# Optimization experiments

Measured on AMD Instinct MI355X. Metric: run time of the kernel, lower is better.

The kernel has to match this reference:

```python
import jax, jax.numpy as jnp
import numpy as np

N, H, B, E = 8192, 64, 8, 262144


def setup_inputs() -> dict:
    key = jax.random.key(0)
    ks = jax.random.split(key, 16)
    inp = {
        "x": jax.random.uniform(ks[0], (B, N, 2), dtype=jnp.float32),
        "edge_index": jax.random.randint(ks[1], (2, E), 0, N, dtype=jnp.int64),
        "target_node": jax.random.randint(ks[2], (B,), 0, N, dtype=jnp.int64),
        "current_prereq_mask": jax.random.uniform(ks[3], (B, N), dtype=jnp.float32),
        # learned parameters (eval mode: dropout is identity)
        "node_emb": jax.random.normal(ks[4], (N, H), dtype=jnp.float32) * 0.02,
        "W_sp": jax.random.normal(ks[5], (H, 2), dtype=jnp.float32) * 0.5,
        "b_sp": jnp.zeros((H,), dtype=jnp.float32),
        "W_g": jax.random.normal(ks[6], (H, H), dtype=jnp.float32) * (1.0 / np.sqrt(H)),
        "b_g": jnp.zeros((H,), dtype=jnp.float32),
        "W_d": jax.random.normal(ks[7], (1, H), dtype=jnp.float32) * (1.0 / np.sqrt(H)),
        "b_d": jnp.zeros((1,), dtype=jnp.float32),
        "W_a": jax.random.normal(ks[8], (1, H), dtype=jnp.float32) * (1.0 / np.sqrt(H)),
        "b_a": jnp.zeros((1,), dtype=jnp.float32),
        "prereq_w": jnp.array([1.0], dtype=jnp.float32),
    }
    return inp


def _build_adj_norm(edge_index):
    # A_hat = A + I ; adj_norm = D^{-1/2} A_hat D^{-1/2}, dense [N, N]
    adj = jnp.zeros((N, N), dtype=jnp.float32).at[edge_index[0], edge_index[1]].set(1.0)
    adj = adj + jnp.eye(N, dtype=jnp.float32)
    deg = adj.sum(axis=1)
    dis = jnp.where(deg > 0, deg ** -0.5, 0.0)
    return dis[:, None] * adj * dis[None, :]


def reference(x, edge_index, target_node, current_prereq_mask,
              node_emb, W_sp, b_sp, W_g, b_g, W_d, b_d, W_a, b_a, prereq_w):
    adj_norm = _build_adj_norm(edge_index)               # [N, N]
    h = node_emb[None] + x @ W_sp.T + b_sp               # [B, N, H]
    h_proj = h @ W_g.T                                   # [B, N, H]
    z = jnp.einsum('nm,bmh->bnh', adj_norm, h_proj) + b_g
    z = jax.nn.relu(z)                                   # [B, N, H]

    target_emb = jnp.take_along_axis(z, target_node[:, None, None].astype(jnp.int32).repeat(1, axis=1), axis=1)[:, 0, :]  # [B, H]
    difficulty = (target_emb @ W_d.T + b_d)[:, 0]        # [B]

    scores = x[:, :, 1]                                  # [B, N]
    n_learned = jnp.clip(x[:, :, 0].sum(axis=1), 1.0)    # [B]
    weighted_z = jnp.einsum('bnh,bn->bh', z, scores) / n_learned[:, None]
    ability = (weighted_z @ W_a.T + b_a)[:, 0]           # [B]

    z_pos = jax.nn.softplus(z)
    prereq_agg = jnp.einsum('bnh,bn->bh', z_pos, current_prereq_mask).mean(axis=-1)  # [B]
    prereq_strength = jnp.abs(prereq_w)[0] * prereq_agg

    gap = ability - difficulty + prereq_strength
    prob = jax.nn.sigmoid(gap)
    return prob, gap
```

## Files before the change

### kernel.cpp

```cpp
#include <hip/hip_runtime.h>
#include <hip/hip_bf16.h>
#include <math.h>

#define N 8192
#define H 64
#define B 8
#define MAXDEG 128
#define REPS 32
#define RPW 2

#define OFF_MASK 0ULL
#define OFF_CNT  8388608ULL
#define OFF_WR   8421376ULL
#define OFF_PR   8486912ULL
#define OFF_NL   8552448ULL
#define ZERO_END 8552512ULL
#define OFF_COLS 8552512ULL
#define OFF_TGT  10649664ULL
#define OFF_UV   10651712ULL
#define OFF_XD   10652480ULL
#define OFF_PD   11701056ULL

__device__ __forceinline__ float bf2f(unsigned short u) {
    return __uint_as_float(((unsigned)u) << 16);
}

__global__ __launch_bounds__(256) void k_zero(float4* __restrict__ p) {
    unsigned i = blockIdx.x * 256u + threadIdx.x;
    if (i < (unsigned)(ZERO_END / 16))
        p[i] = make_float4(0.f, 0.f, 0.f, 0.f);
}

__global__ __launch_bounds__(256) void k_edges(const int* __restrict__ ei, int nE,
                                               unsigned* __restrict__ bits,
                                               unsigned* __restrict__ cnt,
                                               unsigned short* __restrict__ cols) {
    int e = blockIdx.x * blockDim.x + threadIdx.x;
    if (e >= nE) return;
    int r = ei[e];
    int c = ei[nE + e];
    unsigned bitidx = (unsigned)r * (unsigned)N + (unsigned)c;
    unsigned bit = 1u << (bitidx & 31u);
    unsigned old = atomicOr(&bits[bitidx >> 5], bit);
    if (!(old & bit)) {
        unsigned k = atomicAdd(&cnt[r], 1u);
        if (k < MAXDEG) cols[r * MAXDEG + k] = (unsigned short)c;
    }
}

__global__ __launch_bounds__(256) void k_prepxd(const float* __restrict__ ne,
                                                const float* __restrict__ W_g,
                                                const float* __restrict__ W_sp,
                                                const float* __restrict__ b_sp,
                                                const float* __restrict__ x,
                                                const float* __restrict__ pmask,
                                                const unsigned* __restrict__ cnt,
                                                __hip_bfloat16* __restrict__ Pd,
                                                float* __restrict__ uvec,
                                                float* __restrict__ xd,
                                                float* __restrict__ nlacc) {
    __shared__ float wgs[H * 65];
    __shared__ __align__(16) float hv[16 * H];
    const int tid = threadIdx.x, lane = tid & 63, wv = tid >> 6;
    const int bid = blockIdx.x;

    if (bid < 512) {
        for (int e = tid; e < H * H; e += 256)
            wgs[(e >> 6) * 65 + (e & 63)] = W_g[e];
        const float* nebase = ne + (size_t)bid * 16 * H;
        for (int j = 0; j < 4; ++j) {
            int e = tid + j * 256;
            hv[e] = nebase[e];
        }
        __syncthreads();
        float wr[H];
#pragma unroll
        for (int k = 0; k < H; ++k) wr[k] = wgs[lane * 65 + k];

        if (bid == 0 && wv == 0) {
            float v0 = W_sp[lane * 2 + 0], v1 = W_sp[lane * 2 + 1], vb = b_sp[lane];
            float a0 = 0.f, a1 = 0.f, a2 = 0.f;
#pragma unroll
            for (int k = 0; k < H; ++k) {
                a0 = fmaf(wr[k], __shfl(v0, k, 64), a0);
                a1 = fmaf(wr[k], __shfl(v1, k, 64), a1);
                a2 = fmaf(wr[k], __shfl(vb, k, 64), a2);
            }
            uvec[lane] = a0; uvec[64 + lane] = a1; uvec[128 + lane] = a2;
        }

        for (int ii = 0; ii < 4; ++ii) {
            const int node = wv * 4 + ii;
            const int m = bid * 16 + node;
            const float4* h4p = (const float4*)&hv[node * H];
            float acc = 0.f;
#pragma unroll
            for (int kk = 0; kk < 16; ++kk) {
                float4 h4 = h4p[kk];
                acc = fmaf(wr[4 * kk + 0], h4.x, acc);
                acc = fmaf(wr[4 * kk + 1], h4.y, acc);
                acc = fmaf(wr[4 * kk + 2], h4.z, acc);
                acc = fmaf(wr[4 * kk + 3], h4.w, acc);
            }
            float dis = rsqrtf((float)(cnt[m] + 1u));
            Pd[m * H + lane] = __float2bfloat16(dis * acc);
        }
    } else {
        const int m = (bid - 512) * 256 + tid;
        float dis = rsqrtf((float)(cnt[m] + 1u));
        float row[32];
#pragma unroll
        for (int j = 0; j < 32; ++j) row[j] = 0.f;
        row[16] = dis;
#pragma unroll
        for (int b = 0; b < B; ++b) {
            float2 xv = ((const float2*)x)[b * N + m];
            row[b]      = dis * xv.x;
            row[8 + b]  = dis * xv.y;
            row[17 + b] = pmask[b * N + m];
            float s = xv.x;
            for (int off = 32; off; off >>= 1) s += __shfl_down(s, off, 64);
            if (lane == 0) atomicAdd(&nlacc[b], s);
        }
        float4* dst = (float4*)&xd[m * 32];
#pragma unroll
        for (int j = 0; j < 8; ++j)
            dst[j] = make_float4(row[4 * j], row[4 * j + 1], row[4 * j + 2], row[4 * j + 3]);
    }
}

__global__ __launch_bounds__(256) void k_spmm(const unsigned short* __restrict__ Pd,
                                              const float* __restrict__ xd,
                                              const unsigned* __restrict__ cnt,
                                              const unsigned short* __restrict__ cols,
                                              const float* __restrict__ uvec,
                                              const float* __restrict__ b_g,
                                              const int* __restrict__ target,
                                              float* __restrict__ wr_,
                                              float* __restrict__ pr_,
                                              float* __restrict__ tgt) {
    const int lane = threadIdx.x & 63;
    const int wv = threadIdx.x >> 6;
    const int wid = blockIdx.x * 4 + wv;
    const float u0 = uvec[lane], u1 = uvec[64 + lane], ub = uvec[128 + lane];
    const float bg = b_g[lane];
    int tg[B];
#pragma unroll
    for (int b = 0; b < B; ++b) tg[b] = target[b];
    float wa[B], pa[B];
#pragma unroll
    for (int b = 0; b < B; ++b) { wa[b] = 0.f; pa[b] = 0.f; }

    for (int i = 0; i < RPW; ++i) {
        const int r = wid * RPW + i;
        float rloc = xd[r * 32 + (lane & 31)];
        float sp = bf2f(Pd[r * H + lane]);
        float sx = rloc;
        const int kc = min((int)cnt[r], MAXDEG);
        const unsigned short* cl = &cols[r * MAXDEG];
#pragma unroll 4
        for (int k = 0; k < kc; ++k) {
            int c = (int)cl[k];
            sp += bf2f(Pd[c * H + lane]);
            sx += xd[c * 32 + (lane & 31)];
        }
        const float dis_r = __shfl(rloc, 16, 64);
        const float rdis = 1.0f / dis_r;
        const float sd = __shfl(sx, 16, 64);
        const float base = fmaf(sd, ub, sp);
#pragma unroll
        for (int b = 0; b < B; ++b) {
            float sx0 = __shfl(sx, b, 64);
            float sx1 = __shfl(sx, 8 + b, 64);
            float sc  = __shfl(rloc, 8 + b, 64) * rdis;
            float mk  = __shfl(rloc, 17 + b, 64);
            float v = fmaf(sx0, u0, fmaf(sx1, u1, base));
            float z = fmaxf(fmaf(dis_r, v, bg), 0.f);
            wa[b] = fmaf(z, sc, wa[b]);
            float spl = z + __logf(1.f + __expf(-z));
            pa[b] = fmaf(spl, mk, pa[b]);
            if (r == tg[b]) tgt[b * H + lane] = z;
        }
    }
    const int rep = wid & (REPS - 1);
#pragma unroll
    for (int b = 0; b < B; ++b) {
        atomicAdd(&wr_[(rep * B + b) * H + lane], wa[b]);
        atomicAdd(&pr_[(rep * B + b) * H + lane], pa[b]);
    }
}

__global__ __launch_bounds__(512) void k_final(const float* __restrict__ wr_,
                                               const float* __restrict__ pr_,
                                               const float* __restrict__ nlacc,
                                               const float* __restrict__ tgt,
                                               const float* __restrict__ W_d,
                                               const float* __restrict__ b_d,
                                               const float* __restrict__ W_a,
                                               const float* __restrict__ b_a,
                                               const float* __restrict__ prereq_w,
                                               float* __restrict__ out) {
    int tid = threadIdx.x, b = tid >> 6, h = tid & 63;
    float ws = 0.f, ps = 0.f;
#pragma unroll 8
    for (int rep = 0; rep < REPS; ++rep) {
        ws += wr_[(rep * B + b) * H + h];
        ps += pr_[(rep * B + b) * H + h];
    }
    float nl = fmaxf(nlacc[b], 1.0f);
    float ap = (ws / nl) * W_a[h];
    float dp = tgt[b * H + h] * W_d[h];
    float pp = ps;
    for (int off = 32; off; off >>= 1) {
        ap += __shfl_down(ap, off, 64);
        dp += __shfl_down(dp, off, 64);
        pp += __shfl_down(pp, off, 64);
    }
    if (h == 0) {
        float ability    = ap + b_a[0];
        float difficulty = dp + b_d[0];
        float preq       = fabsf(prereq_w[0]) * (pp * (1.0f / (float)H));
        float gap  = ability - difficulty + preq;
        float prob = 1.0f / (1.0f + __expf(-gap));
        out[b]     = prob;
        out[B + b] = gap;
    }
}

extern "C" void kernel_launch(void* const* d_in, const int* in_sizes, int n_in,
                              void* d_out, int out_size, void* d_ws, size_t ws_size,
                              hipStream_t stream) {
    const float* x        = (const float*)d_in[0];
    const int*   ei       = (const int*)d_in[1];
    const int*   target   = (const int*)d_in[2];
    const float* pmask    = (const float*)d_in[3];
    const float* node_emb = (const float*)d_in[4];
    const float* W_sp     = (const float*)d_in[5];
    const float* b_sp     = (const float*)d_in[6];
    const float* W_g      = (const float*)d_in[7];
    const float* b_g      = (const float*)d_in[8];
    const float* W_d      = (const float*)d_in[9];
    const float* b_d      = (const float*)d_in[10];
    const float* W_a      = (const float*)d_in[11];
    const float* b_a      = (const float*)d_in[12];
    const float* prereq_w = (const float*)d_in[13];

    const int nE = in_sizes[1] / 2;

    char* ws = (char*)d_ws;
    unsigned*        bits = (unsigned*)(ws + OFF_MASK);
    unsigned*        cnt  = (unsigned*)(ws + OFF_CNT);
    float*           wr_  = (float*)(ws + OFF_WR);
    float*           pr_  = (float*)(ws + OFF_PR);
    float*           nlac = (float*)(ws + OFF_NL);
    unsigned short*  cols = (unsigned short*)(ws + OFF_COLS);
    float*           tgt  = (float*)(ws + OFF_TGT);
    float*           uvec = (float*)(ws + OFF_UV);
    float*           xd   = (float*)(ws + OFF_XD);
    __hip_bfloat16*  Pd   = (__hip_bfloat16*)(ws + OFF_PD);

    k_zero<<<(unsigned)(ZERO_END / 16 + 255) / 256, 256, 0, stream>>>((float4*)ws);
    k_edges<<<(nE + 255) / 256, 256, 0, stream>>>(ei, nE, bits, cnt, cols);
    k_prepxd<<<544, 256, 0, stream>>>(node_emb, W_g, W_sp, b_sp, x, pmask, cnt,
                                      Pd, uvec, xd, nlac);
    k_spmm<<<N / (4 * RPW), 256, 0, stream>>>((const unsigned short*)Pd, xd, cnt, cols,
                                              uvec, b_g, target, wr_, pr_, tgt);
    k_final<<<1, 512, 0, stream>>>(wr_, pr_, nlac, tgt, W_d, b_d, W_a, b_a,
                                   prereq_w, (float*)d_out);
}
```

Baseline: 79.16 us.

## Fuse all stages into one persistent kernel with software grid barriers

Replaces the five separate launches (zero, edge insertion, prep, spmm, final) with a single 512-block persistent kernel that separates phases with atomic-counter grid barriers, plus a tiny kernel that resets the barrier counters. The goal is to remove per-launch overhead and the inter-kernel gaps. The partial-sum replica count drops from 32 to 16, and the final reduction is done by block 0 after a completion counter. This relies on all 512 blocks being co-resident, since the spin barriers could deadlock otherwise, and each barrier adds sleep/poll latency.

```diff
diff --git a/kernel.cpp b/kernel.cpp
--- a/kernel.cpp
+++ b/kernel.cpp
@@ -6,73 +6,104 @@
 #define H 64
 #define B 8
 #define MAXDEG 128
-#define REPS 32
-#define RPW 2
+#define REPS 16
+#define NBLK 512
+#define NTHR 256
+#define GSIZE (NBLK * NTHR)
+#define NWAVE (NBLK * 4)
+#define RPW   (N / NWAVE)
 
 #define OFF_MASK 0ULL
 #define OFF_CNT  8388608ULL
 #define OFF_WR   8421376ULL
-#define OFF_PR   8486912ULL
-#define OFF_NL   8552448ULL
-#define ZERO_END 8552512ULL
-#define OFF_COLS 8552512ULL
-#define OFF_TGT  10649664ULL
-#define OFF_UV   10651712ULL
-#define OFF_XD   10652480ULL
-#define OFF_PD   11701056ULL
+#define OFF_PR   8454144ULL
+#define OFF_NL   8486912ULL
+#define ZERO_END 8486976ULL
+#define OFF_BAR  8486976ULL
+#define OFF_COLS 8487040ULL
+#define OFF_TGT  10584192ULL
+#define OFF_UV   10586240ULL
+#define OFF_XD   10587008ULL
+#define OFF_PD   11635584ULL
 
 __device__ __forceinline__ float bf2f(unsigned short u) {
     return __uint_as_float(((unsigned)u) << 16);
 }
 
-__global__ __launch_bounds__(256) void k_zero(float4* __restrict__ p) {
-    unsigned i = blockIdx.x * 256u + threadIdx.x;
-    if (i < (unsigned)(ZERO_END / 16))
-        p[i] = make_float4(0.f, 0.f, 0.f, 0.f);
-}
-
-__global__ __launch_bounds__(256) void k_edges(const int* __restrict__ ei, int nE,
-                                               unsigned* __restrict__ bits,
-                                               unsigned* __restrict__ cnt,
-                                               unsigned short* __restrict__ cols) {
-    int e = blockIdx.x * blockDim.x + threadIdx.x;
-    if (e >= nE) return;
-    int r = ei[e];
-    int c = ei[nE + e];
-    unsigned bitidx = (unsigned)r * (unsigned)N + (unsigned)c;
-    unsigned bit = 1u << (bitidx & 31u);
-    unsigned old = atomicOr(&bits[bitidx >> 5], bit);
-    if (!(old & bit)) {
-        unsigned k = atomicAdd(&cnt[r], 1u);
-        if (k < MAXDEG) cols[r * MAXDEG + k] = (unsigned short)c;
-    }
-}
-
-__global__ __launch_bounds__(256) void k_prepxd(const float* __restrict__ ne,
-                                                const float* __restrict__ W_g,
-                                                const float* __restrict__ W_sp,
-                                                const float* __restrict__ b_sp,
-                                                const float* __restrict__ x,
-                                                const float* __restrict__ pmask,
-                                                const unsigned* __restrict__ cnt,
-                                                __hip_bfloat16* __restrict__ Pd,
-                                                float* __restrict__ uvec,
-                                                float* __restrict__ xd,
-                                                float* __restrict__ nlacc) {
+__device__ __forceinline__ void gbar(unsigned* c) {
+    __syncthreads();
+    if (threadIdx.x == 0) {
+        __hip_atomic_fetch_add(c, 1u, __ATOMIC_ACQ_REL, __HIP_MEMORY_SCOPE_AGENT);
+        while (__hip_atomic_load(c, __ATOMIC_ACQUIRE, __HIP_MEMORY_SCOPE_AGENT) < (unsigned)NBLK)
+            __builtin_amdgcn_s_sleep(2);
+    }
+    __syncthreads();
+}
+
+__global__ __launch_bounds__(64) void k_bar0(unsigned* __restrict__ bar) {
+    if (threadIdx.x < 16) bar[threadIdx.x] = 0u;
+}
+
+__global__ __launch_bounds__(NTHR, 2) void k_fused(
+    const float* __restrict__ x, const int* __restrict__ ei, int nE,
+    const int* __restrict__ target, const float* __restrict__ pmask,
+    const float* __restrict__ ne, const float* __restrict__ W_sp,
+    const float* __restrict__ b_sp, const float* __restrict__ W_g,
+    const float* __restrict__ b_g, const float* __restrict__ W_d,
+    const float* __restrict__ b_d, const float* __restrict__ W_a,
+    const float* __restrict__ b_a, const float* __restrict__ prereq_w,
+    char* __restrict__ ws, float* __restrict__ out)
+{
     __shared__ float wgs[H * 65];
     __shared__ __align__(16) float hv[16 * H];
-    const int tid = threadIdx.x, lane = tid & 63, wv = tid >> 6;
-    const int bid = blockIdx.x;
-
-    if (bid < 512) {
-        for (int e = tid; e < H * H; e += 256)
-            wgs[(e >> 6) * 65 + (e & 63)] = W_g[e];
+
+    unsigned*       bits = (unsigned*)(ws + OFF_MASK);
+    unsigned*       cnt  = (unsigned*)(ws + OFF_CNT);
+    float*          wr_  = (float*)(ws + OFF_WR);
+    float*          pr_  = (float*)(ws + OFF_PR);
+    float*          nlac = (float*)(ws + OFF_NL);
+    unsigned*       bar  = (unsigned*)(ws + OFF_BAR);
+    unsigned short* cols = (unsigned short*)(ws + OFF_COLS);
+    float*          tgt  = (float*)(ws + OFF_TGT);
+    float*          uvec = (float*)(ws + OFF_UV);
+    float*          xd   = (float*)(ws + OFF_XD);
+    __hip_bfloat16* Pd   = (__hip_bfloat16*)(ws + OFF_PD);
+
+    const int tid  = threadIdx.x;
+    const int lane = tid & 63;
+    const int wv   = tid >> 6;
+    const int bid  = blockIdx.x;
+    const int gid  = bid * NTHR + tid;
+    const int wid  = bid * 4 + wv;
+
+    {
+        float4* z = (float4*)ws;
+        const float4 f0 = make_float4(0.f, 0.f, 0.f, 0.f);
+        for (unsigned i = gid; i < (unsigned)(ZERO_END / 16); i += GSIZE) z[i] = f0;
+    }
+    gbar(&bar[0]);
+
+    for (int e = gid; e < nE; e += GSIZE) {
+        int r = ei[e];
+        int c = ei[nE + e];
+        unsigned bitidx = (unsigned)r * (unsigned)N + (unsigned)c;
+        unsigned bit = 1u << (bitidx & 31u);
+        unsigned old = atomicOr(&bits[bitidx >> 5], bit);
+        if (!(old & bit)) {
+            unsigned k = atomicAdd(&cnt[r], 1u);
+            if (k < MAXDEG) cols[r * MAXDEG + k] = (unsigned short)c;
+        }
+    }
+    gbar(&bar[1]);
+
+    for (int e = tid; e < H * H; e += NTHR)
+        wgs[(e >> 6) * 65 + (e & 63)] = W_g[e];
+    {
         const float* nebase = ne + (size_t)bid * 16 * H;
-        for (int j = 0; j < 4; ++j) {
-            int e = tid + j * 256;
-            hv[e] = nebase[e];
-        }
-        __syncthreads();
+        for (int j = 0; j < 4; ++j) hv[tid + j * NTHR] = nebase[tid + j * NTHR];
+    }
+    __syncthreads();
+    {
         float wr[H];
 #pragma unroll
         for (int k = 0; k < H; ++k) wr[k] = wgs[lane * 65 + k];
@@ -105,8 +136,9 @@
             float dis = rsqrtf((float)(cnt[m] + 1u));
             Pd[m * H + lane] = __float2bfloat16(dis * acc);
         }
-    } else {
-        const int m = (bid - 512) * 256 + tid;
+    }
+    if (bid >= NBLK - 32) {
+        const int m = (bid - (NBLK - 32)) * NTHR + tid;
         float dis = rsqrtf((float)(cnt[m] + 1u));
         float row[32];
 #pragma unroll
@@ -120,110 +152,102 @@
             row[17 + b] = pmask[b * N + m];
             float s = xv.x;
             for (int off = 32; off; off >>= 1) s += __shfl_down(s, off, 64);
-            if (lane == 0) atomicAdd(&nlacc[b], s);
+            if (lane == 0) atomicAdd(&nlac[b], s);
         }
         float4* dst = (float4*)&xd[m * 32];
 #pragma unroll
         for (int j = 0; j < 8; ++j)
             dst[j] = make_float4(row[4 * j], row[4 * j + 1], row[4 * j + 2], row[4 * j + 3]);
     }
-}
-
-__global__ __launch_bounds__(256) void k_spmm(const unsigned short* __restrict__ Pd,
-                                              const float* __restrict__ xd,
-                                              const unsigned* __restrict__ cnt,
-                                              const unsigned short* __restrict__ cols,
-                                              const float* __restrict__ uvec,
-                                              const float* __restrict__ b_g,
-                                              const int* __restrict__ target,
-                                              float* __restrict__ wr_,
-                                              float* __restrict__ pr_,
-                                              float* __restrict__ tgt) {
-    const int lane = threadIdx.x & 63;
-    const int wv = threadIdx.x >> 6;
-    const int wid = blockIdx.x * 4 + wv;
-    const float u0 = uvec[lane], u1 = uvec[64 + lane], ub = uvec[128 + lane];
-    const float bg = b_g[lane];
-    int tg[B];
-#pragma unroll
-    for (int b = 0; b < B; ++b) tg[b] = target[b];
-    float wa[B], pa[B];
-#pragma unroll
-    for (int b = 0; b < B; ++b) { wa[b] = 0.f; pa[b] = 0.f; }
-
-    for (int i = 0; i < RPW; ++i) {
-        const int r = wid * RPW + i;
-        float rloc = xd[r * 32 + (lane & 31)];
-        float sp = bf2f(Pd[r * H + lane]);
-        float sx = rloc;
-        const int kc = min((int)cnt[r], MAXDEG);
-        const unsigned short* cl = &cols[r * MAXDEG];
+    gbar(&bar[2]);
+
+    {
+        const float u0 = uvec[lane], u1 = uvec[64 + lane], ub = uvec[128 + lane];
+        const float bg = b_g[lane];
+        int tg[B];
+#pragma unroll
+        for (int b = 0; b < B; ++b) tg[b] = target[b];
+        float wa[B], pa[B];
+#pragma unroll
+        for (int b = 0; b < B; ++b) { wa[b] = 0.f; pa[b] = 0.f; }
+
+        for (int i = 0; i < RPW; ++i) {
+            const int r = wid * RPW + i;
+            float rloc = xd[r * 32 + (lane & 31)];
+            float sp = bf2f(((const unsigned short*)Pd)[r * H + lane]);
+            float sx = rloc;
+            const int kc = min((int)cnt[r], MAXDEG);
+            const unsigned short* cl = &cols[r * MAXDEG];
 #pragma unroll 4
-        for (int k = 0; k < kc; ++k) {
-            int c = (int)cl[k];
-            sp += bf2f(Pd[c * H + lane]);
-            sx += xd[c * 32 + (lane & 31)];
-        }
-        const float dis_r = __shfl(rloc, 16, 64);
-        const float rdis = 1.0f / dis_r;
-        const float sd = __shfl(sx, 16, 64);
-        const float base = fmaf(sd, ub, sp);
+            for (int k = 0; k < kc; ++k) {
+                int c = (int)cl[k];
+                sp += bf2f(((const unsigned short*)Pd)[c * H + lane]);
+                sx += xd[c * 32 + (lane & 31)];
+            }
+            const float dis_r = __shfl(rloc, 16, 64);
+            const float rdis = 1.0f / dis_r;
+            const float sd = __shfl(sx, 16, 64);
+            const float base = fmaf(sd, ub, sp);
+#pragma unroll
+            for (int b = 0; b < B; ++b) {
+                float sx0 = __shfl(sx, b, 64);
+                float sx1 = __shfl(sx, 8 + b, 64);
+                float sc  = __shfl(rloc, 8 + b, 64) * rdis;
+                float mk  = __shfl(rloc, 17 + b, 64);
+                float v = fmaf(sx0, u0, fmaf(sx1, u1, base));
+                float z = fmaxf(fmaf(dis_r, v, bg), 0.f);
+                wa[b] = fmaf(z, sc, wa[b]);
+                float spl = z + __logf(1.f + __expf(-z));
+                pa[b] = fmaf(spl, mk, pa[b]);
+                if (r == tg[b]) tgt[b * H + lane] = z;
+            }
+        }
+        const int rep = wid & (REPS - 1);
 #pragma unroll
         for (int b = 0; b < B; ++b) {
-            float sx0 = __shfl(sx, b, 64);
-            float sx1 = __shfl(sx, 8 + b, 64);
-            float sc  = __shfl(rloc, 8 + b, 64) * rdis;
-            float mk  = __shfl(rloc, 17 + b, 64);
-            float v = fmaf(sx0, u0, fmaf(sx1, u1, base));
-            float z = fmaxf(fmaf(dis_r, v, bg), 0.f);
-            wa[b] = fmaf(z, sc, wa[b]);
-            float spl = z + __logf(1.f + __expf(-z));
-            pa[b] = fmaf(spl, mk, pa[b]);
-            if (r == tg[b]) tgt[b * H + lane] = z;
-        }
-    }
-    const int rep = wid & (REPS - 1);
-#pragma unroll
-    for (int b = 0; b < B; ++b) {
-        atomicAdd(&wr_[(rep * B + b) * H + lane], wa[b]);
-        atomicAdd(&pr_[(rep * B + b) * H + lane], pa[b]);
-    }
-}
-
-__global__ __launch_bounds__(512) void k_final(const float* __restrict__ wr_,
-                                               const float* __restrict__ pr_,
-                                               const float* __restrict__ nlacc,
-                                               const float* __restrict__ tgt,
-                                               const float* __restrict__ W_d,
-                                               const float* __restrict__ b_d,
-                                               const float* __restrict__ W_a,
-                                               const float* __restrict__ b_a,
-                                               const float* __restrict__ prereq_w,
-                                               float* __restrict__ out) {
-    int tid = threadIdx.x, b = tid >> 6, h = tid & 63;
-    float ws = 0.f, ps = 0.f;
-#pragma unroll 8
-    for (int rep = 0; rep < REPS; ++rep) {
-        ws += wr_[(rep * B + b) * H + h];
-        ps += pr_[(rep * B + b) * H + h];
-    }
-    float nl = fmaxf(nlacc[b], 1.0f);
-    float ap = (ws / nl) * W_a[h];
-    float dp = tgt[b * H + h] * W_d[h];
-    float pp = ps;
-    for (int off = 32; off; off >>= 1) {
-        ap += __shfl_down(ap, off, 64);
-        dp += __shfl_down(dp, off, 64);
-        pp += __shfl_down(pp, off, 64);
-    }
-    if (h == 0) {
-        float ability    = ap + b_a[0];
-        float difficulty = dp + b_d[0];
-        float preq       = fabsf(prereq_w[0]) * (pp * (1.0f / (float)H));
-        float gap  = ability - difficulty + preq;
-        float prob = 1.0f / (1.0f + __expf(-gap));
-        out[b]     = prob;
-        out[B + b] = gap;
+            atomicAdd(&wr_[(rep * B + b) * H + lane], wa[b]);
+            atomicAdd(&pr_[(rep * B + b) * H + lane], pa[b]);
+        }
+    }
+
+    __syncthreads();
+    if (tid == 0)
+        __hip_atomic_fetch_add(&bar[3], 1u, __ATOMIC_ACQ_REL, __HIP_MEMORY_SCOPE_AGENT);
+    if (bid != 0) return;
+    if (tid == 0) {
+        while (__hip_atomic_load(&bar[3], __ATOMIC_ACQUIRE, __HIP_MEMORY_SCOPE_AGENT) < (unsigned)NBLK)
+            __builtin_amdgcn_s_sleep(2);
+    }
+    __syncthreads();
+
+    {
+        const int h = lane;
+        for (int bb = wv; bb < B; bb += 4) {
+            float wsum = 0.f, psum = 0.f;
+#pragma unroll
+            for (int rep = 0; rep < REPS; ++rep) {
+                wsum += wr_[(rep * B + bb) * H + h];
+                psum += pr_[(rep * B + bb) * H + h];
+            }
+            float nl = fmaxf(nlac[bb], 1.0f);
+            float ap = (wsum / nl) * W_a[h];
+            float dp = tgt[bb * H + h] * W_d[h];
+            float pp = psum;
+            for (int off = 32; off; off >>= 1) {
+                ap += __shfl_down(ap, off, 64);
+                dp += __shfl_down(dp, off, 64);
+                pp += __shfl_down(pp, off, 64);
+            }
+            if (h == 0) {
+                float ability    = ap + b_a[0];
+                float difficulty = dp + b_d[0];
+                float preq       = fabsf(prereq_w[0]) * (pp * (1.0f / (float)H));
+                float gap  = ability - difficulty + preq;
+                float prob = 1.0f / (1.0f + __expf(-gap));
+                out[bb]     = prob;
+                out[B + bb] = gap;
+            }
+        }
     }
 }
 
@@ -234,7 +258,7 @@
     const int*   ei       = (const int*)d_in[1];
     const int*   target   = (const int*)d_in[2];
     const float* pmask    = (const float*)d_in[3];
-    const float* node_emb = (const float*)d_in[4];
+    const float* ne       = (const float*)d_in[4];
     const float* W_sp     = (const float*)d_in[5];
     const float* b_sp     = (const float*)d_in[6];
     const float* W_g      = (const float*)d_in[7];
@@ -246,25 +270,11 @@
     const float* prereq_w = (const float*)d_in[13];
 
     const int nE = in_sizes[1] / 2;
-
-    char* ws = (char*)d_ws;
-    unsigned*        bits = (unsigned*)(ws + OFF_MASK);
-    unsigned*        cnt  = (unsigned*)(ws + OFF_CNT);
-    float*           wr_  = (float*)(ws + OFF_WR);
-    float*           pr_  = (float*)(ws + OFF_PR);
-    float*           nlac = (float*)(ws + OFF_NL);
-    unsigned short*  cols = (unsigned short*)(ws + OFF_COLS);
-    float*           tgt  = (float*)(ws + OFF_TGT);
-    float*           uvec = (float*)(ws + OFF_UV);
-    float*           xd   = (float*)(ws + OFF_XD);
-    __hip_bfloat16*  Pd   = (__hip_bfloat16*)(ws + OFF_PD);
-
-    k_zero<<<(unsigned)(ZERO_END / 16 + 255) / 256, 256, 0, stream>>>((float4*)ws);
-    k_edges<<<(nE + 255) / 256, 256, 0, stream>>>(ei, nE, bits, cnt, cols);
-    k_prepxd<<<544, 256, 0, stream>>>(node_emb, W_g, W_sp, b_sp, x, pmask, cnt,
-                                      Pd, uvec, xd, nlac);
-    k_spmm<<<N / (4 * RPW), 256, 0, stream>>>((const unsigned short*)Pd, xd, cnt, cols,
-                                              uvec, b_g, target, wr_, pr_, tgt);
-    k_final<<<1, 512, 0, stream>>>(wr_, pr_, nlac, tgt, W_d, b_d, W_a, b_a,
-                                   prereq_w, (float*)d_out);
-}
+    char*  ws  = (char*)d_ws;
+    float* out = (float*)d_out;
+
+    k_bar0<<<1, 64, 0, stream>>>((unsigned*)(ws + OFF_BAR));
+    k_fused<<<NBLK, NTHR, 0, stream>>>(x, ei, nE, target, pmask, ne, W_sp, b_sp,
+                                       W_g, b_g, W_d, b_d, W_a, b_a, prereq_w,
+                                       ws, out);
+}
```

After: 282.7 us. 257% more time.

## Drop dense edge bitmask, dedupe per row, pack fp16 records for SpMM gather

Applied to the files above, without the earlier changes.

Removes the 8 MB dense N×N bitmask, along with the atomicOr dedup and its zeroing, and instead deduplicates each row's column list inside the prep kernel using shared memory, a ballot and a compaction step. Projected embeddings and per-node auxiliary data (scaled x, dis, mask) are packed as fp16 pairs into one 32-bit record per lane, so the SpMM gather fetches one word per neighbour instead of separate bf16 and fp32 arrays. The n_learned reduction moves into the SpMM kernel, and the SpMM now handles one row per wave with two accumulators. fp16 has less range than bf16 and can lose accuracy on large sums. The O(deg) scan per lane in the dedup adds work on rows with high degree.

```diff
diff --git a/kernel.cpp b/kernel.cpp
--- a/kernel.cpp
+++ b/kernel.cpp
@@ -1,29 +1,22 @@
 #include <hip/hip_runtime.h>
-#include <hip/hip_bf16.h>
+#include <hip/hip_fp16.h>
 #include <math.h>
 
 #define N 8192
 #define H 64
 #define B 8
 #define MAXDEG 128
-#define REPS 32
-#define RPW 2
-
-#define OFF_MASK 0ULL
-#define OFF_CNT  8388608ULL
-#define OFF_WR   8421376ULL
-#define OFF_PR   8486912ULL
-#define OFF_NL   8552448ULL
-#define ZERO_END 8552512ULL
-#define OFF_COLS 8552512ULL
-#define OFF_TGT  10649664ULL
-#define OFF_UV   10651712ULL
-#define OFF_XD   10652480ULL
-#define OFF_PD   11701056ULL
-
-__device__ __forceinline__ float bf2f(unsigned short u) {
-    return __uint_as_float(((unsigned)u) << 16);
-}
+#define REPS 16
+
+#define OFF_CNT  0ULL
+#define OFF_WR   32768ULL
+#define OFF_PR   65536ULL
+#define OFF_NLR  98304ULL
+#define ZERO_END 98816ULL
+#define OFF_COLS 98816ULL
+#define OFF_TGT  2195968ULL
+#define OFF_UV   2198016ULL
+#define OFF_REC  2198784ULL
 
 __global__ __launch_bounds__(256) void k_zero(float4* __restrict__ p) {
     unsigned i = blockIdx.x * 256u + threadIdx.x;
@@ -32,105 +25,108 @@
 }
 
 __global__ __launch_bounds__(256) void k_edges(const int* __restrict__ ei, int nE,
-                                               unsigned* __restrict__ bits,
                                                unsigned* __restrict__ cnt,
                                                unsigned short* __restrict__ cols) {
-    int e = blockIdx.x * blockDim.x + threadIdx.x;
+    int e = blockIdx.x * 256 + threadIdx.x;
     if (e >= nE) return;
     int r = ei[e];
     int c = ei[nE + e];
-    unsigned bitidx = (unsigned)r * (unsigned)N + (unsigned)c;
-    unsigned bit = 1u << (bitidx & 31u);
-    unsigned old = atomicOr(&bits[bitidx >> 5], bit);
-    if (!(old & bit)) {
-        unsigned k = atomicAdd(&cnt[r], 1u);
-        if (k < MAXDEG) cols[r * MAXDEG + k] = (unsigned short)c;
-    }
-}
-
-__global__ __launch_bounds__(256) void k_prepxd(const float* __restrict__ ne,
-                                                const float* __restrict__ W_g,
-                                                const float* __restrict__ W_sp,
-                                                const float* __restrict__ b_sp,
-                                                const float* __restrict__ x,
-                                                const float* __restrict__ pmask,
-                                                const unsigned* __restrict__ cnt,
-                                                __hip_bfloat16* __restrict__ Pd,
-                                                float* __restrict__ uvec,
-                                                float* __restrict__ xd,
-                                                float* __restrict__ nlacc) {
+    unsigned k = atomicAdd(&cnt[r], 1u);
+    if (k < MAXDEG) cols[r * MAXDEG + k] = (unsigned short)c;
+}
+
+__global__ __launch_bounds__(256) void k_prep(const float* __restrict__ ne,
+                                              const float* __restrict__ W_g,
+                                              const float* __restrict__ W_sp,
+                                              const float* __restrict__ b_sp,
+                                              const float* __restrict__ x,
+                                              const float* __restrict__ pmask,
+                                              unsigned* __restrict__ cnt,
+                                              unsigned short* __restrict__ cols,
+                                              unsigned* __restrict__ rec,
+                                              float* __restrict__ uvec) {
     __shared__ float wgs[H * 65];
-    __shared__ __align__(16) float hv[16 * H];
+    __shared__ unsigned short ls[4][MAXDEG];
     const int tid = threadIdx.x, lane = tid & 63, wv = tid >> 6;
     const int bid = blockIdx.x;
 
-    if (bid < 512) {
-        for (int e = tid; e < H * H; e += 256)
-            wgs[(e >> 6) * 65 + (e & 63)] = W_g[e];
-        const float* nebase = ne + (size_t)bid * 16 * H;
-        for (int j = 0; j < 4; ++j) {
-            int e = tid + j * 256;
-            hv[e] = nebase[e];
-        }
-        __syncthreads();
-        float wr[H];
-#pragma unroll
-        for (int k = 0; k < H; ++k) wr[k] = wgs[lane * 65 + k];
-
-        if (bid == 0 && wv == 0) {
-            float v0 = W_sp[lane * 2 + 0], v1 = W_sp[lane * 2 + 1], vb = b_sp[lane];
-            float a0 = 0.f, a1 = 0.f, a2 = 0.f;
-#pragma unroll
-            for (int k = 0; k < H; ++k) {
-                a0 = fmaf(wr[k], __shfl(v0, k, 64), a0);
-                a1 = fmaf(wr[k], __shfl(v1, k, 64), a1);
-                a2 = fmaf(wr[k], __shfl(vb, k, 64), a2);
-            }
-            uvec[lane] = a0; uvec[64 + lane] = a1; uvec[128 + lane] = a2;
-        }
-
-        for (int ii = 0; ii < 4; ++ii) {
-            const int node = wv * 4 + ii;
-            const int m = bid * 16 + node;
-            const float4* h4p = (const float4*)&hv[node * H];
-            float acc = 0.f;
-#pragma unroll
-            for (int kk = 0; kk < 16; ++kk) {
-                float4 h4 = h4p[kk];
-                acc = fmaf(wr[4 * kk + 0], h4.x, acc);
-                acc = fmaf(wr[4 * kk + 1], h4.y, acc);
-                acc = fmaf(wr[4 * kk + 2], h4.z, acc);
-                acc = fmaf(wr[4 * kk + 3], h4.w, acc);
-            }
-            float dis = rsqrtf((float)(cnt[m] + 1u));
-            Pd[m * H + lane] = __float2bfloat16(dis * acc);
-        }
-    } else {
-        const int m = (bid - 512) * 256 + tid;
-        float dis = rsqrtf((float)(cnt[m] + 1u));
-        float row[32];
-#pragma unroll
-        for (int j = 0; j < 32; ++j) row[j] = 0.f;
-        row[16] = dis;
-#pragma unroll
-        for (int b = 0; b < B; ++b) {
-            float2 xv = ((const float2*)x)[b * N + m];
-            row[b]      = dis * xv.x;
-            row[8 + b]  = dis * xv.y;
-            row[17 + b] = pmask[b * N + m];
-            float s = xv.x;
-            for (int off = 32; off; off >>= 1) s += __shfl_down(s, off, 64);
-            if (lane == 0) atomicAdd(&nlacc[b], s);
-        }
-        float4* dst = (float4*)&xd[m * 32];
-#pragma unroll
-        for (int j = 0; j < 8; ++j)
-            dst[j] = make_float4(row[4 * j], row[4 * j + 1], row[4 * j + 2], row[4 * j + 3]);
-    }
-}
-
-__global__ __launch_bounds__(256) void k_spmm(const unsigned short* __restrict__ Pd,
-                                              const float* __restrict__ xd,
+    for (int e = tid; e < H * H; e += 256)
+        wgs[(e >> 6) * 65 + (e & 63)] = W_g[e];
+    __syncthreads();
+
+    float wr[H];
+#pragma unroll
+    for (int k = 0; k < H; ++k) wr[k] = wgs[lane * 65 + k];
+
+    if (bid == 0 && wv == 0) {
+        float v0 = W_sp[lane * 2 + 0], v1 = W_sp[lane * 2 + 1], vb = b_sp[lane];
+        float a0 = 0.f, a1 = 0.f, a2 = 0.f;
+#pragma unroll
+        for (int k = 0; k < H; ++k) {
+            a0 = fmaf(wr[k], __shfl(v0, k, 64), a0);
+            a1 = fmaf(wr[k], __shfl(v1, k, 64), a1);
+            a2 = fmaf(wr[k], __shfl(vb, k, 64), a2);
+        }
+        uvec[lane] = a0; uvec[64 + lane] = a1; uvec[128 + lane] = a2;
+    }
+
+    for (int i = 0; i < 2; ++i) {
+        const int r = (bid * 4 + wv) * 2 + i;
+        const int kraw = min((int)cnt[r], MAXDEG);
+        unsigned short* cl = &cols[r * MAXDEG];
+        for (int t = lane; t < kraw; t += 64) ls[wv][t] = cl[t];
+        int c0 = (lane < kraw) ? (int)ls[wv][lane] : -1;
+        int dup0 = 0;
+        for (int j = 0; j < lane && j < kraw; ++j)
+            dup0 |= ((int)ls[wv][j] == c0);
+        unsigned long long m0 = __ballot((lane < kraw) && !dup0);
+        unsigned long long below = (1ULL << lane) - 1ULL;
+        unsigned tot = __popcll(m0);
+        if ((lane < kraw) && !dup0)
+            cl[__popcll(m0 & below)] = (unsigned short)c0;
+        if (kraw > 64) {
+            const int i1 = lane + 64;
+            int c1 = (i1 < kraw) ? (int)ls[wv][i1] : -2;
+            int dup1 = 0;
+            for (int j = 0; j < i1 && j < kraw; ++j)
+                dup1 |= ((int)ls[wv][j] == c1);
+            unsigned long long m1 = __ballot((i1 < kraw) && !dup1);
+            if ((i1 < kraw) && !dup1)
+                cl[tot + __popcll(m1 & below)] = (unsigned short)c1;
+            tot += __popcll(m1);
+        }
+        if (lane == 0) cnt[r] = tot;
+        const float dis = rsqrtf((float)(tot + 1u));
+
+        float xvx = 0.f, xvy = 0.f, pm = 0.f;
+        if (lane < 8) {
+            float2 t2 = ((const float2*)x)[lane * N + r];
+            xvx = t2.x; xvy = t2.y;
+        }
+        if (lane >= 17 && lane < 25) pm = pmask[(lane - 17) * N + r];
+        float yv = __shfl(xvy, lane & 7, 64);
+        float aux = (lane < 8)   ? dis * xvx
+                  : (lane < 16)  ? dis * yv
+                  : (lane == 16) ? dis
+                  : (lane < 25)  ? pm : 0.f;
+
+        const float4* ne4 = (const float4*)(ne + (size_t)r * H);
+        float acc = 0.f;
+#pragma unroll
+        for (int kk = 0; kk < 16; ++kk) {
+            float4 h4 = ne4[kk];
+            acc = fmaf(wr[4 * kk + 0], h4.x, acc);
+            acc = fmaf(wr[4 * kk + 1], h4.y, acc);
+            acc = fmaf(wr[4 * kk + 2], h4.z, acc);
+            acc = fmaf(wr[4 * kk + 3], h4.w, acc);
+        }
+        unsigned w = ((unsigned)__half_as_ushort(__float2half(dis * acc)) << 16)
+                   |  (unsigned)__half_as_ushort(__float2half(aux));
+        rec[(size_t)r * 64 + lane] = w;
+    }
+}
+
+__global__ __launch_bounds__(256) void k_spmm(const unsigned* __restrict__ rec,
                                               const unsigned* __restrict__ cnt,
                                               const unsigned short* __restrict__ cols,
                                               const float* __restrict__ uvec,
@@ -138,61 +134,71 @@
                                               const int* __restrict__ target,
                                               float* __restrict__ wr_,
                                               float* __restrict__ pr_,
+                                              float* __restrict__ nlr,
                                               float* __restrict__ tgt) {
-    const int lane = threadIdx.x & 63;
-    const int wv = threadIdx.x >> 6;
-    const int wid = blockIdx.x * 4 + wv;
+    const int lane = threadIdx.x & 63, wv = threadIdx.x >> 6;
+    const int r = blockIdx.x * 4 + wv;
     const float u0 = uvec[lane], u1 = uvec[64 + lane], ub = uvec[128 + lane];
     const float bg = b_g[lane];
     int tg[B];
 #pragma unroll
     for (int b = 0; b < B; ++b) tg[b] = target[b];
+
+    const unsigned vown = rec[(size_t)r * 64 + lane];
+    float2 fown = __half22float2(*(const __half2*)&vown);
+
+    float spA = fown.y, sxA = fown.x, spB = 0.f, sxB = 0.f;
+    const int kc = min((int)cnt[r], MAXDEG);
+    const unsigned short* cl = &cols[r * MAXDEG];
+    int k = 0;
+#pragma unroll 2
+    for (; k + 2 <= kc; k += 2) {
+        int cA = cl[k], cB = cl[k + 1];
+        unsigned vA = rec[(size_t)cA * 64 + lane];
+        unsigned vB = rec[(size_t)cB * 64 + lane];
+        float2 fA = __half22float2(*(const __half2*)&vA);
+        float2 fB = __half22float2(*(const __half2*)&vB);
+        spA += fA.y; sxA += fA.x;
+        spB += fB.y; sxB += fB.x;
+    }
+    if (k < kc) {
+        int c = cl[k];
+        unsigned v = rec[(size_t)c * 64 + lane];
+        float2 f = __half22float2(*(const __half2*)&v);
+        spA += f.y; sxA += f.x;
+    }
+    const float sp = spA + spB;
+    const float sx = sxA + sxB;
+
+    const float dis_r = __shfl(fown.x, 16, 64);
+    const float rdis = 1.0f / dis_r;
+    const float sd = __shfl(sx, 16, 64);
+    const float base = fmaf(sd, ub, sp);
     float wa[B], pa[B];
 #pragma unroll
-    for (int b = 0; b < B; ++b) { wa[b] = 0.f; pa[b] = 0.f; }
-
-    for (int i = 0; i < RPW; ++i) {
-        const int r = wid * RPW + i;
-        float rloc = xd[r * 32 + (lane & 31)];
-        float sp = bf2f(Pd[r * H + lane]);
-        float sx = rloc;
-        const int kc = min((int)cnt[r], MAXDEG);
-        const unsigned short* cl = &cols[r * MAXDEG];
-#pragma unroll 4
-        for (int k = 0; k < kc; ++k) {
-            int c = (int)cl[k];
-            sp += bf2f(Pd[c * H + lane]);
-            sx += xd[c * 32 + (lane & 31)];
-        }
-        const float dis_r = __shfl(rloc, 16, 64);
-        const float rdis = 1.0f / dis_r;
-        const float sd = __shfl(sx, 16, 64);
-        const float base = fmaf(sd, ub, sp);
-#pragma unroll
-        for (int b = 0; b < B; ++b) {
-            float sx0 = __shfl(sx, b, 64);
-            float sx1 = __shfl(sx, 8 + b, 64);
-            float sc  = __shfl(rloc, 8 + b, 64) * rdis;
-            float mk  = __shfl(rloc, 17 + b, 64);
-            float v = fmaf(sx0, u0, fmaf(sx1, u1, base));
-            float z = fmaxf(fmaf(dis_r, v, bg), 0.f);
-            wa[b] = fmaf(z, sc, wa[b]);
-            float spl = z + __logf(1.f + __expf(-z));
-            pa[b] = fmaf(spl, mk, pa[b]);
-            if (r == tg[b]) tgt[b * H + lane] = z;
-        }
-    }
-    const int rep = wid & (REPS - 1);
+    for (int b = 0; b < B; ++b) {
+        float sx0 = __shfl(sx, b, 64);
+        float sx1 = __shfl(sx, 8 + b, 64);
+        float sc  = __shfl(fown.x, 8 + b, 64) * rdis;
+        float mk  = __shfl(fown.x, 17 + b, 64);
+        float v = fmaf(sx0, u0, fmaf(sx1, u1, base));
+        float z = fmaxf(fmaf(dis_r, v, bg), 0.f);
+        wa[b] = z * sc;
+        pa[b] = (z + __logf(1.f + __expf(-z))) * mk;
+        if (r == tg[b]) tgt[b * H + lane] = z;
+    }
+    const int rep = r & (REPS - 1);
 #pragma unroll
     for (int b = 0; b < B; ++b) {
         atomicAdd(&wr_[(rep * B + b) * H + lane], wa[b]);
         atomicAdd(&pr_[(rep * B + b) * H + lane], pa[b]);
     }
+    if (lane < 8) atomicAdd(&nlr[rep * 8 + lane], fown.x * rdis);
 }
 
 __global__ __launch_bounds__(512) void k_final(const float* __restrict__ wr_,
                                                const float* __restrict__ pr_,
-                                               const float* __restrict__ nlacc,
+                                               const float* __restrict__ nlr,
                                                const float* __restrict__ tgt,
                                                const float* __restrict__ W_d,
                                                const float* __restrict__ b_d,
@@ -201,13 +207,14 @@
                                                const float* __restrict__ prereq_w,
                                                float* __restrict__ out) {
     int tid = threadIdx.x, b = tid >> 6, h = tid & 63;
-    float ws = 0.f, ps = 0.f;
-#pragma unroll 8
+    float ws = 0.f, ps = 0.f, nlv = 0.f;
+#pragma unroll
     for (int rep = 0; rep < REPS; ++rep) {
-        ws += wr_[(rep * B + b) * H + h];
-        ps += pr_[(rep * B + b) * H + h];
-    }
-    float nl = fmaxf(nlacc[b], 1.0f);
+        ws  += wr_[(rep * B + b) * H + h];
+        ps  += pr_[(rep * B + b) * H + h];
+        nlv += nlr[rep * 8 + b];
+    }
+    float nl = fmaxf(nlv, 1.0f);
     float ap = (ws / nl) * W_a[h];
     float dp = tgt[b * H + h] * W_d[h];
     float pp = ps;
@@ -234,7 +241,7 @@
     const int*   ei       = (const int*)d_in[1];
     const int*   target   = (const int*)d_in[2];
     const float* pmask    = (const float*)d_in[3];
-    const float* node_emb = (const float*)d_in[4];
+    const float* ne       = (const float*)d_in[4];
     const float* W_sp     = (const float*)d_in[5];
     const float* b_sp     = (const float*)d_in[6];
     const float* W_g      = (const float*)d_in[7];
@@ -248,23 +255,21 @@
     const int nE = in_sizes[1] / 2;
 
     char* ws = (char*)d_ws;
-    unsigned*        bits = (unsigned*)(ws + OFF_MASK);
     unsigned*        cnt  = (unsigned*)(ws + OFF_CNT);
     float*           wr_  = (float*)(ws + OFF_WR);
     float*           pr_  = (float*)(ws + OFF_PR);
-    float*           nlac = (float*)(ws + OFF_NL);
+    float*           nlr  = (float*)(ws + OFF_NLR);
     unsigned short*  cols = (unsigned short*)(ws + OFF_COLS);
     float*           tgt  = (float*)(ws + OFF_TGT);
     float*           uvec = (float*)(ws + OFF_UV);
-    float*           xd   = (float*)(ws + OFF_XD);
-    __hip_bfloat16*  Pd   = (__hip_bfloat16*)(ws + OFF_PD);
+    unsigned*        rec  = (unsigned*)(ws + OFF_REC);
 
     k_zero<<<(unsigned)(ZERO_END / 16 + 255) / 256, 256, 0, stream>>>((float4*)ws);
-    k_edges<<<(nE + 255) / 256, 256, 0, stream>>>(ei, nE, bits, cnt, cols);
-    k_prepxd<<<544, 256, 0, stream>>>(node_emb, W_g, W_sp, b_sp, x, pmask, cnt,
-                                      Pd, uvec, xd, nlac);
-    k_spmm<<<N / (4 * RPW), 256, 0, stream>>>((const unsigned short*)Pd, xd, cnt, cols,
-                                              uvec, b_g, target, wr_, pr_, tgt);
-    k_final<<<1, 512, 0, stream>>>(wr_, pr_, nlac, tgt, W_d, b_d, W_a, b_a,
+    k_edges<<<(nE + 255) / 256, 256, 0, stream>>>(ei, nE, cnt, cols);
+    k_prep<<<N / 8, 256, 0, stream>>>(ne, W_g, W_sp, b_sp, x, pmask, cnt, cols,
+                                      rec, uvec);
+    k_spmm<<<N / 4, 256, 0, stream>>>(rec, cnt, cols, uvec, b_g, target,
+                                      wr_, pr_, nlr, tgt);
+    k_final<<<1, 512, 0, stream>>>(wr_, pr_, nlr, tgt, W_d, b_d, W_a, b_a,
                                    prereq_w, (float*)d_out);
 }
```

Result: slower. 93.51 us (+18.1%).
